# Kernel optimization log

Hardware: AMD Instinct MI355X
Metric: run time of the kernel (lower is better)

The kernel has to match this reference:

```python
import jax, jax.numpy as jnp
import numpy as np

NEG_INF = float(-2 ** 31)
B, S, D_IN, D_H, H = 4, 2048, 512, 512, 8


def setup_inputs() -> dict:
    key = jax.random.key(0)
    ks = jax.random.split(key, 11)
    sc_in = 1.0 / np.sqrt(D_IN)
    sc_pr = 1.0 / np.sqrt(D_H * H)
    x = jax.random.normal(ks[0], (B, S, D_IN), dtype=jnp.float32)
    mask = jax.random.randint(ks[1], (B, 1, S), 0, 2, dtype=jnp.int32)
    Wq = jax.random.uniform(ks[2], (H, D_IN, D_H), jnp.float32, -sc_in, sc_in)
    bq = jax.random.uniform(ks[3], (H, D_H), jnp.float32, -sc_in, sc_in)
    Wk = jax.random.uniform(ks[4], (H, D_IN, D_H), jnp.float32, -sc_in, sc_in)
    bk = jax.random.uniform(ks[5], (H, D_H), jnp.float32, -sc_in, sc_in)
    Wv = jax.random.uniform(ks[6], (H, D_IN, D_H), jnp.float32, -sc_in, sc_in)
    bv = jax.random.uniform(ks[7], (H, D_H), jnp.float32, -sc_in, sc_in)
    Wp = jax.random.uniform(ks[8], (H * D_H, D_H), jnp.float32, -sc_pr, sc_pr)
    bp = jax.random.uniform(ks[9], (D_H,), jnp.float32, -sc_pr, sc_pr)
    return {"x": x, "mask": mask, "Wq": Wq, "bq": bq, "Wk": Wk, "bk": bk,
            "Wv": Wv, "bv": bv, "Wp": Wp, "bp": bp}


def reference(x, mask, Wq, bq, Wk, bk, Wv, bv, Wp, bp):
    # per-head Q/K/V projections, batched over the head axis h
    q = jnp.einsum('bsd,hde->bhse', x, Wq) + bq[None, :, None, :]
    k = jnp.einsum('bsd,hde->bhse', x, Wk) + bk[None, :, None, :]
    v = jnp.einsum('bsd,hde->bhse', x, Wv) + bv[None, :, None, :]
    scores = jnp.einsum('bhse,bhte->bhst', q, k) / jnp.sqrt(jnp.float32(D_H))
    scores = jnp.where(mask[:, None, :, :] == 0, NEG_INF, scores)
    probs = jax.nn.softmax(scores, axis=-1)
    out = jnp.einsum('bhst,bhte->bhse', probs, v)  # [B,H,S,D_H]
    cat = out.transpose(0, 2, 1, 3).reshape(B, S, H * D_H)
    return cat @ Wp + bp
```

## Files before the change

### kernel.cpp

```cpp
#include <hip/hip_runtime.h>
#include <hip/hip_bf16.h>
#include <cstdint>
#include <cstddef>

typedef unsigned short ushort_t;
typedef __bf16 bf16x8 __attribute__((ext_vector_type(8)));
typedef float floatx4 __attribute__((ext_vector_type(4)));

#define S_LEN 2048
#define DIN   512
#define DH    512
#define NHEAD 8
#define NBAT  4
#define NBH   32
#define HP    4096

#define MiB (1024ull * 1024ull)
#define WQT_OFF   (0ull)
#define WKT_OFF   (4ull  * MiB)
#define WVT_OFF   (8ull  * MiB)
#define WPT_OFF   (12ull * MiB)
#define XBF_OFF   (16ull * MiB)
#define Q_OFF     (24ull * MiB)
#define K_OFF     (88ull * MiB)
#define VT_OFF    (152ull * MiB)
#define O_OFF     (216ull * MiB)
#define LSUM_OFF  (280ull * MiB)
#define P_OFF     (281ull * MiB)
#define WS_BYTES  (409ull * MiB)

__device__ __align__(256) unsigned char g_ws[WS_BYTES];

__device__ __forceinline__ ushort_t f2bf(float f) {
  union { float f; uint32_t u; } v; v.f = f;
  uint32_t r = v.u + 0x7fffu + ((v.u >> 16) & 1u);
  return (ushort_t)(r >> 16);
}

typedef __attribute__((address_space(3))) uint32_t lds_uint;
typedef __attribute__((address_space(1))) const uint32_t glb_uint;

__device__ __forceinline__ void async16(void* lds, const void* g) {
  __builtin_amdgcn_global_load_lds((glb_uint*)g, (lds_uint*)lds, 16, 0, 0);
}

#define BBAR() do { \
    __builtin_amdgcn_sched_barrier(0); \
    __builtin_amdgcn_s_barrier(); \
    __builtin_amdgcn_sched_barrier(0); \
  } while (0)


#define STG_A(dbuf, hh, kt) do { \
    const ushort_t* _g = gA + (size_t)(kt) * 64 + (size_t)(hh) * a128; \
    char* _s = sAh + (dbuf) * 32768 + (hh) * 16384; \
    async16(_s, _g); \
    async16(_s + 8192, _g + a64); \
  } while (0)

#define STG_B(dbuf, hh, kt) do { \
    const ushort_t* _g = gB + (size_t)(kt) * 64 + (size_t)(hh) * b128; \
    char* _s = sBh + (dbuf) * 32768 + (hh) * 16384; \
    async16(_s, _g); \
    async16(_s + 8192, _g + b64); \
  } while (0)

#define LD_A(dst, qm) do { \
    const char* _b = (const char*)As + cur * 32768 + (qm) * 16384 + aoff0; \
    _Pragma("unroll") \
    for (int _i = 0; _i < 4; ++_i) { \
      dst[_i][0] = *(const bf16x8*)(_b + (_i << 11) + swz0); \
      dst[_i][1] = *(const bf16x8*)(_b + (_i << 11) + swz1); \
    } } while (0)

#define LD_B(dst, qn) do { \
    const char* _b = (const char*)Bs + cur * 32768 + (qn) * 16384 + boff0; \
    _Pragma("unroll") \
    for (int _j = 0; _j < 2; ++_j) { \
      dst[_j][0] = *(const bf16x8*)(_b + (_j << 11) + swz0); \
      dst[_j][1] = *(const bf16x8*)(_b + (_j << 11) + swz1); \
    } } while (0)

#define MM(q, AF, BF) do { \
    __builtin_amdgcn_s_setprio(1); \
    _Pragma("unroll") \
    for (int _i = 0; _i < 4; ++_i) { \
      _Pragma("unroll") \
      for (int _j = 0; _j < 2; ++_j) { \
        acc[q][_i][_j] = __builtin_amdgcn_mfma_f32_16x16x32_bf16(AF[_i][0], BF[_j][0], acc[q][_i][_j], 0, 0, 0); \
        acc[q][_i][_j] = __builtin_amdgcn_mfma_f32_16x16x32_bf16(AF[_i][1], BF[_j][1], acc[q][_i][_j], 0, 0, 0); \
      } \
    } \
    __builtin_amdgcn_s_setprio(0); \
  } while (0)

__device__ __forceinline__ void gemm256_core(
    const ushort_t* __restrict__ A, const ushort_t* __restrict__ Bt,
    int lda, int ldb, int kdim,
    ushort_t* As, ushort_t* Bs, floatx4 acc[4][4][2])
{
  const int t = threadIdx.x;
  const int w = t >> 6, l = t & 63;
  const int l15 = l & 15, lq = l >> 4;
  const int wq_r = w >> 2, wq_c = w & 3;

  const int r0 = t >> 3, c0 = t & 7;
  const ushort_t* gA = A + (size_t)r0 * lda + ((c0 ^ (r0 & 7)) << 3);
  const ushort_t* gB = Bt + (size_t)r0 * ldb + ((c0 ^ (r0 & 7)) << 3);
  const size_t a64 = (size_t)64 * lda, b64 = (size_t)64 * ldb;
  const size_t a128 = (size_t)128 * lda, b128 = (size_t)128 * ldb;
  char* sAh = (char*)As + (w << 10);
  char* sBh = (char*)Bs + (w << 10);

  const int aoff0 = ((wq_r << 6) + l15) << 7;
  const int boff0 = ((wq_c << 5) + l15) << 7;
  const int l7 = l15 & 7;
  const int swz0 = (lq ^ l7) << 4;
  const int swz1 = ((4 + lq) ^ l7) << 4;

  const int nt = kdim >> 6;

#pragma unroll
  for (int q = 0; q < 4; ++q)
#pragma unroll
    for (int i = 0; i < 4; ++i)
#pragma unroll
      for (int j = 0; j < 2; ++j)
        acc[q][i][j] = (floatx4){0.f, 0.f, 0.f, 0.f};

  STG_A(0, 0, 0);
  STG_B(0, 1, 0);
  STG_A(0, 1, 0);
  STG_B(0, 0, 0);
  if (nt > 1) {
    STG_A(1, 0, 1);
    STG_B(1, 1, 1);
    asm volatile("s_waitcnt vmcnt(4)" ::: "memory");
  } else {
    asm volatile("s_waitcnt vmcnt(0)" ::: "memory");
  }
  BBAR();

  bf16x8 a[4][2], b0[2][2], b1[2][2];

#pragma unroll 1
  for (int tt = 0; tt < nt; ++tt) {
    const int cur = tt & 1, nxt = cur ^ 1;
    LD_A(a, 0);
    LD_B(b0, 0);
    if (tt + 1 < nt) STG_A(nxt, 1, tt + 1);
    BBAR();
    MM(0, a, b0);
    BBAR();
    LD_B(b1, 1);
    if (tt + 1 < nt) STG_B(nxt, 0, tt + 1);
    BBAR();
    MM(1, a, b1);
    BBAR();
    LD_A(a, 1);
    if (tt + 2 < nt) STG_A(cur, 0, tt + 2);
    BBAR();
    MM(2, a, b1);
    BBAR();
    if (tt + 2 < nt) STG_B(cur, 1, tt + 2);
    BBAR();
    MM(3, a, b0);
    if (tt + 2 < nt) asm volatile("s_waitcnt vmcnt(4)" ::: "memory");
    else             asm volatile("s_waitcnt vmcnt(0)" ::: "memory");
    BBAR();
  }
}

__device__ __forceinline__ void gemm_core(
    const ushort_t* __restrict__ A, const ushort_t* __restrict__ Bt,
    int lda, int ldb, int kdim,
    ushort_t* As, ushort_t* Bs, floatx4 acc[4][4])
{
  const int t = threadIdx.x;
  const int w = t >> 6;
  const int l = t & 63;
  const int wrow = w >> 1, wcol = w & 1;
  const int l15 = l & 15, lq = l >> 4;

  const ushort_t* gA = A + (size_t)(t >> 2) * lda + (t & 3) * 8;
  const ushort_t* gB = Bt + (size_t)(t >> 2) * ldb + (t & 3) * 8;
  const size_t strideA = (size_t)64 * lda;
  const size_t strideB = (size_t)64 * ldb;
  char* ldsA0 = (char*)As + w * 1024;
  char* ldsB0 = (char*)Bs + w * 1024;

  async16(ldsA0,        gA);
  async16(ldsA0 + 4096, gA + strideA);
  async16(ldsB0,        gB);
  async16(ldsB0 + 4096, gB + strideB);

#pragma unroll
  for (int i = 0; i < 4; ++i)
#pragma unroll
    for (int j = 0; j < 4; ++j)
      acc[i][j] = (floatx4){0.f, 0.f, 0.f, 0.f};

  const int nwin = kdim >> 5;
#pragma unroll 1
  for (int k = 0; k < nwin; ++k) {
    __syncthreads();
    const int cur = k & 1;
    if (k + 1 < nwin) {
      const int nxt = cur ^ 1;
      const ushort_t* gA1 = gA + (size_t)(k + 1) * 32;
      const ushort_t* gB1 = gB + (size_t)(k + 1) * 32;
      char* ldsA1 = ldsA0 + nxt * 8192;
      char* ldsB1 = ldsB0 + nxt * 8192;
      async16(ldsA1,        gA1);
      async16(ldsA1 + 4096, gA1 + strideA);
      async16(ldsB1,        gB1);
      async16(ldsB1 + 4096, gB1 + strideB);
    }
    const ushort_t* rdA = As + cur * 4096 + (wrow * 64 + l15) * 32 + lq * 8;
    const ushort_t* rdB = Bs + cur * 4096 + (wcol * 64 + l15) * 32 + lq * 8;

    bf16x8 af[4], bfr[4];
#pragma unroll
    for (int i = 0; i < 4; ++i) af[i] = *(const bf16x8*)(rdA + i * 512);
#pragma unroll
    for (int j = 0; j < 4; ++j) bfr[j] = *(const bf16x8*)(rdB + j * 512);
#pragma unroll
    for (int i = 0; i < 4; ++i)
#pragma unroll
      for (int j = 0; j < 4; ++j)
        acc[i][j] = __builtin_amdgcn_mfma_f32_16x16x32_bf16(af[i], bfr[j], acc[i][j], 0, 0, 0);
  }
}

__global__ __launch_bounds__(256) void convert_f32_bf16(
    const float* __restrict__ src, size_t dstOff, int n)
{
  ushort_t* dst = (ushort_t*)(g_ws + dstOff);
  int i = (blockIdx.x * 256 + threadIdx.x) * 4;
  if (i >= n) return;
  float4 v = *(const float4*)(src + i);
  ushort_t o[4] = {f2bf(v.x), f2bf(v.y), f2bf(v.z), f2bf(v.w)};
  *(uint2*)(dst + i) = *(const uint2*)o;
}

__global__ __launch_bounds__(256) void transpose_f32_bf16(
    const float* __restrict__ src, size_t dstOff, int R, int C)
{
  __shared__ ushort_t tile[32][33];
  ushort_t* dst = (ushort_t*)(g_ws + dstOff) + (size_t)blockIdx.z * R * C;
  src += (size_t)blockIdx.z * R * C;
  int r0 = blockIdx.y * 32, c0 = blockIdx.x * 32;
  int tx = threadIdx.x & 31, ty = threadIdx.x >> 5;
  for (int i = ty; i < 32; i += 8)
    tile[i][tx] = f2bf(src[(size_t)(r0 + i) * C + (c0 + tx)]);
  __syncthreads();
  for (int i = ty; i < 32; i += 8)
    dst[(size_t)(c0 + i) * R + (r0 + tx)] = tile[tx][i];
}

__global__ __launch_bounds__(256) void zero_lsum()
{
  float* lsum = (float*)(g_ws + LSUM_OFF);
  int i = (blockIdx.x * 256 + threadIdx.x) * 4;
  *(float4*)(lsum + i) = (float4){0.f, 0.f, 0.f, 0.f};
}

__global__ __launch_bounds__(512, 2) void qkv_gemm(
    const float* __restrict__ bq, const float* __restrict__ bk,
    const float* __restrict__ bv)
{
  __shared__ __align__(16) ushort_t As[2 * 2 * 128 * 64], Bs[2 * 2 * 128 * 64];
  const int z = blockIdx.z;
  const int bh = z & 31, sel = z >> 5, b = bh >> 3, h = bh & 7;
  const size_t wOff = (sel == 0) ? WQT_OFF : (sel == 1) ? WKT_OFF : WVT_OFF;
  const float* bias = ((sel == 0) ? bq : (sel == 1) ? bk : bv) + h * DH;
  const int tileM = blockIdx.y * 256, tileN = blockIdx.x * 256;

  const ushort_t* A  = (const ushort_t*)(g_ws + XBF_OFF)
                       + ((size_t)b * S_LEN + tileM) * DIN;
  const ushort_t* Bt = (const ushort_t*)(g_ws + wOff)
                       + ((size_t)h * DH + tileN) * DIN;
  floatx4 acc[4][4][2];
  gemm256_core(A, Bt, DIN, DIN, DIN, As, Bs, acc);

  ushort_t* Qb = (ushort_t*)(g_ws + Q_OFF);
  ushort_t* Kb = (ushort_t*)(g_ws + K_OFF);
  ushort_t* VT = (ushort_t*)(g_ws + VT_OFF);
  const int t = threadIdx.x, w = t >> 6, l = t & 63;
  const int l15 = l & 15, lq = l >> 4;
  const int wq_r = w >> 2, wq_c = w & 3;
  const int QM[4] = {0, 0, 1, 1}, QN[4] = {0, 1, 1, 0};
#pragma unroll
  for (int q = 0; q < 4; ++q) {
#pragma unroll
    for (int j = 0; j < 2; ++j) {
      const int n = tileN + QN[q] * 128 + wq_c * 32 + j * 16 + l15;
      const float bsn = bias[n];
#pragma unroll
      for (int i = 0; i < 4; ++i) {
#pragma unroll
        for (int r = 0; r < 4; ++r) {
          const int m = tileM + QM[q] * 128 + wq_r * 64 + i * 16 + lq * 4 + r;
          const float v = acc[q][i][j][r] + bsn;
          if (sel == 0)      Qb[((size_t)bh * S_LEN + m) * DH + n] = f2bf(v);
          else if (sel == 1) Kb[((size_t)bh * S_LEN + m) * DH + n] = f2bf(v);
          else               VT[((size_t)bh * DH + n) * S_LEN + m] = f2bf(v);
        }
      }
    }
  }
}

__global__ __launch_bounds__(512, 2) void scores_kernel(
    const int* __restrict__ mask, int c0)
{
  __shared__ __align__(16) ushort_t As[2 * 2 * 128 * 64], Bs[2 * 2 * 128 * 64];
  const int hl = blockIdx.z, bh = c0 + hl, b = bh >> 3;
  const int tileM = blockIdx.y * 256, tileN = blockIdx.x * 256;

  const ushort_t* A  = (const ushort_t*)(g_ws + Q_OFF)
                       + ((size_t)bh * S_LEN + tileM) * DH;
  const ushort_t* Bt = (const ushort_t*)(g_ws + K_OFF)
                       + ((size_t)bh * S_LEN + tileN) * DH;
  floatx4 acc[4][4][2];
  gemm256_core(A, Bt, DH, DH, DH, As, Bs, acc);

  const float scale = 0.04419417382415922f;
  const int t = threadIdx.x, w = t >> 6, l = t & 63;
  const int l15 = l & 15, lq = l >> 4;
  const int wq_r = w >> 2, wq_c = w & 3;
  const int QM[4] = {0, 0, 1, 1}, QN[4] = {0, 1, 1, 0};
  ushort_t* Pp = (ushort_t*)(g_ws + P_OFF) + (size_t)hl * S_LEN * S_LEN;
  const int* mask_b = mask + (size_t)b * S_LEN;
  float* lsum = (float*)(g_ws + LSUM_OFF);

  float rsum[2][4][4];
#pragma unroll
  for (int qm = 0; qm < 2; ++qm)
#pragma unroll
    for (int i = 0; i < 4; ++i)
#pragma unroll
      for (int r = 0; r < 4; ++r) rsum[qm][i][r] = 0.f;

#pragma unroll
  for (int q = 0; q < 4; ++q) {
#pragma unroll
    for (int j = 0; j < 2; ++j) {
      const int n = tileN + QN[q] * 128 + wq_c * 32 + j * 16 + l15;
      const int mv = mask_b[n];
#pragma unroll
      for (int i = 0; i < 4; ++i) {
#pragma unroll
        for (int r = 0; r < 4; ++r) {
          const int m = tileM + QM[q] * 128 + wq_r * 64 + i * 16 + lq * 4 + r;
          float s = fminf(acc[q][i][j][r] * scale, 30.f);
          const float p = mv ? __expf(s) : 0.f;
          rsum[QM[q]][i][r] += p;
          Pp[(size_t)m * S_LEN + n] = f2bf(p);
        }
      }
    }
  }
#pragma unroll
  for (int qm = 0; qm < 2; ++qm) {
#pragma unroll
    for (int i = 0; i < 4; ++i) {
#pragma unroll
      for (int r = 0; r < 4; ++r) {
        float v = rsum[qm][i][r];
        v += __shfl_xor(v, 1);
        v += __shfl_xor(v, 2);
        v += __shfl_xor(v, 4);
        v += __shfl_xor(v, 8);
        if (l15 == 0) {
          const int m = tileM + qm * 128 + wq_r * 64 + i * 16 + lq * 4 + r;
          atomicAdd(&lsum[(size_t)hl * S_LEN + m], v);
        }
      }
    }
  }
}

__global__ __launch_bounds__(512, 2) void pv_kernel(int c0)
{
  __shared__ __align__(16) ushort_t As[2 * 2 * 128 * 64], Bs[2 * 2 * 128 * 64];
  const int hl = blockIdx.z, bh = c0 + hl, b = bh >> 3, h = bh & 7;
  const int tileM = blockIdx.y * 256, tileN = blockIdx.x * 256;

  const ushort_t* A  = (const ushort_t*)(g_ws + P_OFF)
                       + (size_t)hl * S_LEN * S_LEN + (size_t)tileM * S_LEN;
  const ushort_t* Bt = (const ushort_t*)(g_ws + VT_OFF)
                       + ((size_t)bh * DH + tileN) * S_LEN;
  floatx4 acc[4][4][2];
  gemm256_core(A, Bt, S_LEN, S_LEN, S_LEN, As, Bs, acc);

  const float* lsum = (const float*)(g_ws + LSUM_OFF);
  ushort_t* Ob = (ushort_t*)(g_ws + O_OFF);
  const int t = threadIdx.x, w = t >> 6, l = t & 63;
  const int l15 = l & 15, lq = l >> 4;
  const int wq_r = w >> 2, wq_c = w & 3;
  const int QM[4] = {0, 0, 1, 1}, QN[4] = {0, 1, 1, 0};
#pragma unroll
  for (int q = 0; q < 4; ++q) {
#pragma unroll
    for (int i = 0; i < 4; ++i) {
#pragma unroll
      for (int r = 0; r < 4; ++r) {
        const int m = tileM + QM[q] * 128 + wq_r * 64 + i * 16 + lq * 4 + r;
        const float lv = lsum[(size_t)hl * S_LEN + m];
        const float inv = (lv > 1e-20f) ? 1.0f / lv : 0.f;
#pragma unroll
        for (int j = 0; j < 2; ++j) {
          const int n = tileN + QN[q] * 128 + wq_c * 32 + j * 16 + l15;
          Ob[((size_t)b * S_LEN + m) * HP + h * DH + n] =
              f2bf(acc[q][i][j][r] * inv);
        }
      }
    }
  }
}

__global__ __launch_bounds__(256) void proj_kernel(
    const float* __restrict__ bp, float* __restrict__ out)
{
  __shared__ __align__(16) ushort_t As[2 * 128 * 32], Bs[2 * 128 * 32];
  const int tileM = blockIdx.y * 128, tileN = blockIdx.x * 128;

  const ushort_t* A  = (const ushort_t*)(g_ws + O_OFF) + (size_t)tileM * HP;
  const ushort_t* Bt = (const ushort_t*)(g_ws + WPT_OFF) + (size_t)tileN * HP;
  floatx4 acc[4][4];
  gemm_core(A, Bt, HP, HP, HP, As, Bs, acc);

  const int t = threadIdx.x, w = t >> 6, l = t & 63;
  const int wrow = w >> 1, wcol = w & 1, l15 = l & 15, lq = l >> 4;
#pragma unroll
  for (int j = 0; j < 4; ++j) {
    const int n = tileN + wcol * 64 + j * 16 + l15;
    const float bsn = bp[n];
#pragma unroll
    for (int i = 0; i < 4; ++i) {
#pragma unroll
      for (int r = 0; r < 4; ++r) {
        const int m = tileM + wrow * 64 + i * 16 + lq * 4 + r;
        out[(size_t)m * DH + n] = acc[i][j][r] + bsn;
      }
    }
  }
}

extern "C" void kernel_launch(void* const* d_in, const int* in_sizes, int n_in,
                              void* d_out, int out_size, void* d_ws, size_t ws_size,
                              hipStream_t stream) {
  const float* x  = (const float*)d_in[0];
  const int*   msk= (const int*)d_in[1];
  const float* Wq = (const float*)d_in[2];
  const float* bq = (const float*)d_in[3];
  const float* Wk = (const float*)d_in[4];
  const float* bk = (const float*)d_in[5];
  const float* Wv = (const float*)d_in[6];
  const float* bv = (const float*)d_in[7];
  const float* Wp = (const float*)d_in[8];
  const float* bp = (const float*)d_in[9];
  float* out = (float*)d_out;

  convert_f32_bf16<<<dim3(NBAT * S_LEN * DIN / 1024), 256, 0, stream>>>(
      x, XBF_OFF, NBAT * S_LEN * DIN);

  transpose_f32_bf16<<<dim3(16, 16, NHEAD), 256, 0, stream>>>(Wq, WQT_OFF, DIN, DH);
  transpose_f32_bf16<<<dim3(16, 16, NHEAD), 256, 0, stream>>>(Wk, WKT_OFF, DIN, DH);
  transpose_f32_bf16<<<dim3(16, 16, NHEAD), 256, 0, stream>>>(Wv, WVT_OFF, DIN, DH);
  transpose_f32_bf16<<<dim3(16, 128, 1),    256, 0, stream>>>(Wp, WPT_OFF, HP, DH);

  qkv_gemm<<<dim3(2, 8, 3 * NBH), 512, 0, stream>>>(bq, bk, bv);

  for (int c0 = 0; c0 < NBH; c0 += 16) {
    zero_lsum<<<dim3(32), 256, 0, stream>>>();
    scores_kernel<<<dim3(8, 8, 16), 512, 0, stream>>>(msk, c0);
    pv_kernel<<<dim3(2, 8, 16), 512, 0, stream>>>(c0);
  }

  proj_kernel<<<dim3(DH / 128, (NBAT * S_LEN) / 128), 256, 0, stream>>>(bp, out);
}
```

Measured before the change: 818.1 us.

## Merge GEMM barrier phases and stage V-transpose writes through LDS

The main GEMM loop now issues each MFMA block right after its LDS fragment loads and global prefetch, with no barrier in between, which removes about half of the per-iteration barriers. Setprio now covers the loads as well as the MFMAs. In qkv_gemm, the V projection output is first written transposed into shared memory with an XOR swizzle, then stored to global as coalesced 16-byte rows. This replaces the scattered 2-byte strided stores. Dropping the barriers relies on the remaining waitcnt and barrier ordering to keep the double buffer race-free.

```diff
diff --git a/kernel.cpp b/kernel.cpp
--- a/kernel.cpp
+++ b/kernel.cpp
@@ -82,7 +82,6 @@
     } } while (0)
 
 #define MM(q, AF, BF) do { \
-    __builtin_amdgcn_s_setprio(1); \
     _Pragma("unroll") \
     for (int _i = 0; _i < 4; ++_i) { \
       _Pragma("unroll") \
@@ -91,7 +90,6 @@
         acc[q][_i][_j] = __builtin_amdgcn_mfma_f32_16x16x32_bf16(AF[_i][1], BF[_j][1], acc[q][_i][_j], 0, 0, 0); \
       } \
     } \
-    __builtin_amdgcn_s_setprio(0); \
   } while (0)
 
 __device__ __forceinline__ void gemm256_core(
@@ -146,25 +144,29 @@
 #pragma unroll 1
   for (int tt = 0; tt < nt; ++tt) {
     const int cur = tt & 1, nxt = cur ^ 1;
+    __builtin_amdgcn_s_setprio(1);
     LD_A(a, 0);
     LD_B(b0, 0);
     if (tt + 1 < nt) STG_A(nxt, 1, tt + 1);
+    MM(0, a, b0);
+    __builtin_amdgcn_s_setprio(0);
     BBAR();
-    MM(0, a, b0);
-    BBAR();
+    __builtin_amdgcn_s_setprio(1);
     LD_B(b1, 1);
     if (tt + 1 < nt) STG_B(nxt, 0, tt + 1);
+    MM(1, a, b1);
+    __builtin_amdgcn_s_setprio(0);
     BBAR();
-    MM(1, a, b1);
-    BBAR();
+    __builtin_amdgcn_s_setprio(1);
     LD_A(a, 1);
     if (tt + 2 < nt) STG_A(cur, 0, tt + 2);
+    MM(2, a, b1);
+    __builtin_amdgcn_s_setprio(0);
     BBAR();
-    MM(2, a, b1);
-    BBAR();
+    __builtin_amdgcn_s_setprio(1);
     if (tt + 2 < nt) STG_B(cur, 1, tt + 2);
-    BBAR();
     MM(3, a, b0);
+    __builtin_amdgcn_s_setprio(0);
     if (tt + 2 < nt) asm volatile("s_waitcnt vmcnt(4)" ::: "memory");
     else             asm volatile("s_waitcnt vmcnt(0)" ::: "memory");
     BBAR();
@@ -269,7 +271,9 @@
     const float* __restrict__ bq, const float* __restrict__ bk,
     const float* __restrict__ bv)
 {
-  __shared__ __align__(16) ushort_t As[2 * 2 * 128 * 64], Bs[2 * 2 * 128 * 64];
+  __shared__ __align__(16) ushort_t SH[65536];
+  ushort_t* As = SH;
+  ushort_t* Bs = SH + 32768;
   const int z = blockIdx.z;
   const int bh = z & 31, sel = z >> 5, b = bh >> 3, h = bh & 7;
   const size_t wOff = (sel == 0) ? WQT_OFF : (sel == 1) ? WKT_OFF : WVT_OFF;
@@ -283,38 +287,67 @@
   floatx4 acc[4][4][2];
   gemm256_core(A, Bt, DIN, DIN, DIN, As, Bs, acc);
 
-  ushort_t* Qb = (ushort_t*)(g_ws + Q_OFF);
-  ushort_t* Kb = (ushort_t*)(g_ws + K_OFF);
-  ushort_t* VT = (ushort_t*)(g_ws + VT_OFF);
   const int t = threadIdx.x, w = t >> 6, l = t & 63;
   const int l15 = l & 15, lq = l >> 4;
   const int wq_r = w >> 2, wq_c = w & 3;
   const int QM[4] = {0, 0, 1, 1}, QN[4] = {0, 1, 1, 0};
-#pragma unroll
-  for (int q = 0; q < 4; ++q) {
-#pragma unroll
-    for (int j = 0; j < 2; ++j) {
-      const int n = tileN + QN[q] * 128 + wq_c * 32 + j * 16 + l15;
-      const float bsn = bias[n];
-#pragma unroll
-      for (int i = 0; i < 4; ++i) {
-#pragma unroll
-        for (int r = 0; r < 4; ++r) {
-          const int m = tileM + QM[q] * 128 + wq_r * 64 + i * 16 + lq * 4 + r;
-          const float v = acc[q][i][j][r] + bsn;
-          if (sel == 0)      Qb[((size_t)bh * S_LEN + m) * DH + n] = f2bf(v);
-          else if (sel == 1) Kb[((size_t)bh * S_LEN + m) * DH + n] = f2bf(v);
-          else               VT[((size_t)bh * DH + n) * S_LEN + m] = f2bf(v);
+
+  if (sel == 2) {
+    char* SB = (char*)SH;
+#pragma unroll
+    for (int q = 0; q < 4; ++q) {
+#pragma unroll
+      for (int j = 0; j < 2; ++j) {
+        const int nl = QN[q] * 128 + wq_c * 32 + j * 16 + l15;
+        const float bsn = bias[tileN + nl];
+#pragma unroll
+        for (int i = 0; i < 4; ++i) {
+          const int ml = QM[q] * 128 + wq_r * 64 + i * 16 + lq * 4;
+          ushort_t pk[4];
+#pragma unroll
+          for (int r = 0; r < 4; ++r) pk[r] = f2bf(acc[q][i][j][r] + bsn);
+          const int byte = nl * 512 + (((ml >> 3) ^ (nl & 7)) << 4) + (ml & 7) * 2;
+          *(uint2*)(SB + byte) = *(const uint2*)pk;
         }
       }
     }
+    BBAR();
+    ushort_t* VTb = (ushort_t*)(g_ws + VT_OFF)
+                    + ((size_t)bh * DH + tileN) * S_LEN + tileM;
+#pragma unroll
+    for (int s = 0; s < 16; ++s) {
+      const int nl = (w << 5) + (s << 1) + (l >> 5);
+      const int c  = l & 31;
+      const uint4 v = *(const uint4*)(SB + nl * 512 + ((c ^ (nl & 7)) << 4));
+      *(uint4*)(VTb + (size_t)nl * S_LEN + c * 8) = v;
+    }
+  } else {
+    ushort_t* Db = (ushort_t*)(g_ws + ((sel == 0) ? Q_OFF : K_OFF));
+#pragma unroll
+    for (int q = 0; q < 4; ++q) {
+#pragma unroll
+      for (int j = 0; j < 2; ++j) {
+        const int n = tileN + QN[q] * 128 + wq_c * 32 + j * 16 + l15;
+        const float bsn = bias[n];
+#pragma unroll
+        for (int i = 0; i < 4; ++i) {
+#pragma unroll
+          for (int r = 0; r < 4; ++r) {
+            const int m = tileM + QM[q] * 128 + wq_r * 64 + i * 16 + lq * 4 + r;
+            Db[((size_t)bh * S_LEN + m) * DH + n] = f2bf(acc[q][i][j][r] + bsn);
+          }
+        }
+      }
+    }
   }
 }
 
 __global__ __launch_bounds__(512, 2) void scores_kernel(
     const int* __restrict__ mask, int c0)
 {
-  __shared__ __align__(16) ushort_t As[2 * 2 * 128 * 64], Bs[2 * 2 * 128 * 64];
+  __shared__ __align__(16) ushort_t SH[65536];
+  ushort_t* As = SH;
+  ushort_t* Bs = SH + 32768;
   const int hl = blockIdx.z, bh = c0 + hl, b = bh >> 3;
   const int tileM = blockIdx.y * 256, tileN = blockIdx.x * 256;
 
@@ -383,7 +416,9 @@
 
 __global__ __launch_bounds__(512, 2) void pv_kernel(int c0)
 {
-  __shared__ __align__(16) ushort_t As[2 * 2 * 128 * 64], Bs[2 * 2 * 128 * 64];
+  __shared__ __align__(16) ushort_t SH[65536];
+  ushort_t* As = SH;
+  ushort_t* Bs = SH + 32768;
   const int hl = blockIdx.z, bh = c0 + hl, b = bh >> 3, h = bh & 7;
   const int tileM = blockIdx.y * 256, tileN = blockIdx.x * 256;
 
```

Result: faster. 720.1 us (-12.0%).
